# Kernel optimization log

Measured on AMD Instinct MI355X. Metric: run time of the kernel, lower is better.

The kernel has to match this reference:

```python
import jax, jax.numpy as jnp
import numpy as np

N, D = 8192, 512


def setup_inputs() -> dict:
    key = jax.random.key(0)
    ks = jax.random.split(key, 4)
    scale = 1.0 / np.sqrt(D)
    x = jax.random.normal(ks[0], (N, D), dtype=jnp.float32)
    Wq = jax.random.normal(ks[1], (D, D), dtype=jnp.float32) * scale
    Wk = jax.random.normal(ks[2], (D, D), dtype=jnp.float32) * scale
    Wv = jax.random.normal(ks[3], (D, D), dtype=jnp.float32) * scale
    bq = jnp.zeros((D,), dtype=jnp.float32)
    bk = jnp.zeros((D,), dtype=jnp.float32)
    bv = jnp.zeros((D,), dtype=jnp.float32)
    # causal additive mask: 0 on/below diagonal, -1e9 above
    mask = jnp.where(jnp.arange(N)[:, None] >= jnp.arange(N)[None, :], 0.0, -1e9).astype(jnp.float32)
    return {"x": x, "mask": mask, "Wq": Wq, "bq": bq, "Wk": Wk, "bk": bk, "Wv": Wv, "bv": bv}


def reference(x, mask, Wq, bq, Wk, bk, Wv, bv):
    # torch Linear: y = x @ W.T + b
    q = x @ Wq.T + bq  # [N, D]
    k = x @ Wk.T + bk  # [N, D]
    v = x @ Wv.T + bv  # [N, D]
    inv_sqrt_d = 1.0 / jnp.sqrt(jnp.asarray(D, dtype=x.dtype))
    scores = q @ k.T * inv_sqrt_d + mask          # [N, N] -- the HBM-heavy intermediate
    attention = jax.nn.softmax(scores, axis=-1)   # softmax over key axis
    weighted = attention @ v                       # [N, D]
    return weighted
```

## Files before the change

### kernel.cpp

```cpp
#include <hip/hip_runtime.h>
#include <hip/hip_bf16.h>
#include <stdint.h>


#define N_TOK 8192
#define DIM   512
#define NQB   128
#define CCH   12
#define MAXCH 11
#define NCHTOT 748

typedef __attribute__((ext_vector_type(8))) short bfrag;
typedef __attribute__((ext_vector_type(4))) float facc;
typedef __attribute__((ext_vector_type(4))) unsigned short us4v;
typedef __attribute__((ext_vector_type(2))) float f32x2v;

#define MFMA16(a, b, c) __builtin_amdgcn_mfma_f32_16x16x32_bf16((a), (b), (c), 0, 0, 0)

__device__ __forceinline__ unsigned short f2bf(float f) {
    union { float f; unsigned int u; } v; v.f = f;
    unsigned int r = v.u + 0x7fffu + ((v.u >> 16) & 1u);
    return (unsigned short)(r >> 16);
}
__device__ __forceinline__ float bf2f(unsigned int bits16) {
    union { unsigned int u; float f; } v; v.u = bits16 << 16;
    return v.f;
}
__device__ __forceinline__ void cp16(const unsigned short* g, const unsigned short* l) {
    __builtin_amdgcn_global_load_lds(
        (const __attribute__((address_space(1))) void*)g,
        (__attribute__((address_space(3))) void*)l, 16, 0, 0);
}

__device__ __forceinline__ int part_idx(int qb, int c) {
    return qb + 122 * c - 6 * c * c;
}

__global__ void cvt_x_kernel(const float* __restrict__ src,
                             unsigned short* __restrict__ dst, int n4) {
    int i = blockIdx.x * blockDim.x + threadIdx.x;
    if (i >= n4) return;
    float4 v = ((const float4*)src)[i];
    us4v o; o[0] = f2bf(v.x); o[1] = f2bf(v.y); o[2] = f2bf(v.z); o[3] = f2bf(v.w);
    ((us4v*)dst)[i] = o;
}

__global__ void cvt_w_kernel(const float* __restrict__ wq,
                             const float* __restrict__ wk,
                             const float* __restrict__ wv,
                             unsigned short* __restrict__ dst) {
    int i = blockIdx.x * blockDim.x + threadIdx.x;
    int g = i >> 16;
    int o = i & 65535;
    const float* s = (g == 0) ? wq : (g == 1) ? wk : wv;
    float4 v = ((const float4*)s)[o];
    us4v p; p[0] = f2bf(v.x); p[1] = f2bf(v.y); p[2] = f2bf(v.z); p[3] = f2bf(v.w);
    ((us4v*)dst)[i] = p;
}

__global__ __launch_bounds__(256, 2) void qkv_gemm(
    const unsigned short* __restrict__ xb,
    const unsigned short* __restrict__ wb,
    const float* __restrict__ biasq, const float* __restrict__ biask,
    const float* __restrict__ biasv,
    unsigned short* __restrict__ Qb, unsigned short* __restrict__ Kb,
    unsigned short* __restrict__ VTb) {
    const int z    = blockIdx.z;
    const int tid  = threadIdx.x;
    const int lane = tid & 63;
    const int w    = tid >> 6;
    const int wr   = w >> 1, wc = w & 1;
    const int r0   = blockIdx.x * 128;
    const int c0   = blockIdx.y * 128;
    const unsigned short* wmat = wb + z * 262144;
    const float* bias = (z == 0) ? biasq : (z == 1) ? biask : biasv;
    const int lr  = lane & 15;
    const int lkc = lane >> 4;

    __shared__ unsigned short AB[2][2][128 * 64];

    const int st_row = w * 8 + (lane >> 3);
    const int st_gs  = ((lane & 7) ^ (lane >> 3)) * 8;
    auto stage = [&](int step, int buf) {
        const int kb = step * 64;
#pragma unroll
        for (int i = 0; i < 4; ++i) {
            const int r = i * 32 + st_row;
            cp16(xb   + (size_t)(r0 + r) * 512 + kb + st_gs,
                 &AB[0][buf][(i * 256 + w * 64) * 8]);
            cp16(wmat + (size_t)(c0 + r) * 512 + kb + st_gs,
                 &AB[1][buf][(i * 256 + w * 64) * 8]);
        }
    };

    facc acc[4][4] = {};
    stage(0, 0);
    __syncthreads();

    int buf = 0;
    for (int step = 0; step < 8; ++step) {
        if (step + 1 < 8) stage(step + 1, buf ^ 1);
        bfrag af[4][2], bf4[4][2];
#pragma unroll
        for (int i = 0; i < 4; ++i) {
            const int m = wr * 64 + i * 16 + lr;
            const int mb = m * 64, m7 = m & 7;
            af[i][0] = *(const bfrag*)&AB[0][buf][mb + ((lkc) ^ m7) * 8];
            af[i][1] = *(const bfrag*)&AB[0][buf][mb + ((4 + lkc) ^ m7) * 8];
        }
#pragma unroll
        for (int j = 0; j < 4; ++j) {
            const int n = wc * 64 + j * 16 + lr;
            const int nb = n * 64, n7 = n & 7;
            bf4[j][0] = *(const bfrag*)&AB[1][buf][nb + ((lkc) ^ n7) * 8];
            bf4[j][1] = *(const bfrag*)&AB[1][buf][nb + ((4 + lkc) ^ n7) * 8];
        }
#pragma unroll
        for (int kk = 0; kk < 2; ++kk)
#pragma unroll
            for (int i = 0; i < 4; ++i)
#pragma unroll
                for (int j = 0; j < 4; ++j)
                    acc[i][j] = MFMA16(af[i][kk], bf4[j][kk], acc[i][j]);
        __syncthreads();
        buf ^= 1;
    }

    if (z < 2) {
        unsigned short* out = (z == 0) ? Qb : Kb;
#pragma unroll
        for (int i = 0; i < 4; ++i)
#pragma unroll
            for (int j = 0; j < 4; ++j) {
                const int col = c0 + wc * 64 + j * 16 + lr;
                const float bv_ = bias[col];
#pragma unroll
                for (int r = 0; r < 4; ++r) {
                    const int row = r0 + wr * 64 + i * 16 + lkc * 4 + r;
                    out[(size_t)row * 512 + col] = f2bf(acc[i][j][r] + bv_);
                }
            }
    } else {
#pragma unroll
        for (int i = 0; i < 4; ++i)
#pragma unroll
            for (int j = 0; j < 4; ++j) {
                const int col = c0 + wc * 64 + j * 16 + lr;
                const float bv_ = bias[col];
                us4v pk;
#pragma unroll
                for (int r = 0; r < 4; ++r) pk[r] = f2bf(acc[i][j][r] + bv_);
                *(us4v*)(VTb + (size_t)col * 8192 + (r0 + wr * 64 + i * 16 + lkc * 4)) = pk;
            }
    }
}

__global__ __launch_bounds__(512, 2) void attn_partial(
    const unsigned short* __restrict__ Qb, const unsigned short* __restrict__ Kb,
    const unsigned short* __restrict__ VTb,
    unsigned short* __restrict__ Opart, float* __restrict__ ml) {
    const int hb   = blockIdx.x;
    const int xcd  = hb & 7, pos = hb >> 3;
    const int idx  = (xcd < 4 ? xcd * 94 : 376 + (xcd - 4) * 93) + pos;
    int c = 0;
#pragma unroll
    for (int cc = 1; cc < MAXCH; ++cc)
        if (idx >= 134 * cc - 6 * cc * cc) c = cc;
    const int qb  = 12 * c + (idx - (134 * c - 6 * c * c));
    const int kb0 = c * CCH;
    const int kb1 = min(kb0 + CCH, qb + 1);

    const int tid  = threadIdx.x;
    const int lane = tid & 63;
    const int wv   = tid >> 6;
    const int sr   = wv & 3;
    const int ch   = wv >> 2;
    const int lr   = lane & 15;
    const int lkc  = lane >> 4;
    const int lk   = lkc * 8;
    const int qrow0 = qb * 64;

    __shared__ unsigned short Klds[2][64 * 512];
    __shared__ float          S_lds[64][65];
    __shared__ unsigned short P_lds[64][72];
    __shared__ float m_lds[64], l_lds[64], sc_lds[64];

    if (tid < 64) { m_lds[tid] = -1e30f; l_lds[tid] = 0.f; }

    auto stage_k = [&](int kb, int buf) {
        const unsigned short* src = Kb + (size_t)kb * (64 * 512) + (lane ^ wv) * 8;
#pragma unroll
        for (int i = 0; i < 8; ++i) {
            const int rl = wv + 8 * i;
            cp16(src + (size_t)rl * 512, &Klds[buf][rl * 512]);
        }
    };

    bfrag q[16];
    {
        const unsigned short* qp = Qb + (size_t)(qrow0 + sr * 16 + lr) * 512 + lk;
#pragma unroll
        for (int s = 0; s < 16; ++s) q[s] = *(const bfrag*)(qp + s * 32);
    }
    facc o[4][4] = {};
    stage_k(kb0, 0);
    __syncthreads();

    const int row = tid >> 3;
    const int sub = tid & 7;
    const float sm_scale = 0.044194173824159216f;
    int cur = 0;

    for (int kb = kb0; kb < kb1; ++kb) {
        const int cb = kb * 64;
        if (kb + 1 < kb1) stage_k(kb + 1, cur ^ 1);
        bfrag vbf[2][4];
#pragma unroll
        for (int s = 0; s < 2; ++s)
#pragma unroll
            for (int j = 0; j < 4; ++j)
                vbf[s][j] = *(const bfrag*)(VTb + (size_t)(wv * 64 + j * 16 + lr) * 8192
                                            + cb + s * 32 + lk);
#pragma unroll
        for (int tc = 0; tc < 2; ++tc) {
            facc sa0 = {}, sa1 = {};
            const int rl = ch * 32 + tc * 16 + lr;
            const unsigned short* kbase = &Klds[cur][rl * 512];
            const int rx = rl & 7;
#pragma unroll
            for (int s = 0; s < 16; s += 2) {
                const int sl0 = (s * 4 + lkc) ^ rx;
                const int sl1 = ((s + 1) * 4 + lkc) ^ rx;
                sa0 = MFMA16(q[s],     *(const bfrag*)(kbase + sl0 * 8), sa0);
                sa1 = MFMA16(q[s + 1], *(const bfrag*)(kbase + sl1 * 8), sa1);
            }
#pragma unroll
            for (int r = 0; r < 4; ++r)
                S_lds[sr * 16 + lkc * 4 + r][ch * 32 + tc * 16 + lr] = sa0[r] + sa1[r];
        }
        __syncthreads();

        {
            const int grow  = qrow0 + row;
            const bool diag = (kb == qb);
            float sv[8];
#pragma unroll
            for (int j = 0; j < 8; ++j) {
                float v = S_lds[row][sub * 8 + j] * sm_scale;
                if (diag && (cb + sub * 8 + j > grow)) v = -1e30f;
                sv[j] = v;
            }
            float mx = sv[0];
#pragma unroll
            for (int j = 1; j < 8; ++j) mx = fmaxf(mx, sv[j]);
            mx = fmaxf(mx, __shfl_xor(mx, 1));
            mx = fmaxf(mx, __shfl_xor(mx, 2));
            mx = fmaxf(mx, __shfl_xor(mx, 4));
            const float m_old = m_lds[row];
            const float m_new = fmaxf(m_old, mx);
            float sum = 0.f;
            bfrag pv_;
#pragma unroll
            for (int j = 0; j < 8; ++j) {
                float p = __expf(sv[j] - m_new);
                sum += p;
                pv_[j] = (short)f2bf(p);
            }
            sum += __shfl_xor(sum, 1);
            sum += __shfl_xor(sum, 2);
            sum += __shfl_xor(sum, 4);
            if (sub == 0) {
                const float scl = __expf(m_old - m_new);
                sc_lds[row] = scl;
                m_lds[row]  = m_new;
                l_lds[row]  = l_lds[row] * scl + sum;
            }
            *(bfrag*)(&P_lds[row][sub * 8]) = pv_;
        }
        __syncthreads();

#pragma unroll
        for (int i = 0; i < 4; ++i) {
            float s0 = sc_lds[i * 16 + lkc * 4 + 0];
            float s1 = sc_lds[i * 16 + lkc * 4 + 1];
            float s2 = sc_lds[i * 16 + lkc * 4 + 2];
            float s3 = sc_lds[i * 16 + lkc * 4 + 3];
#pragma unroll
            for (int j = 0; j < 4; ++j) {
                o[i][j][0] *= s0; o[i][j][1] *= s1;
                o[i][j][2] *= s2; o[i][j][3] *= s3;
            }
        }
#pragma unroll
        for (int s = 0; s < 2; ++s) {
            bfrag pa[4];
#pragma unroll
            for (int i = 0; i < 4; ++i)
                pa[i] = *(const bfrag*)(&P_lds[i * 16 + lr][s * 32 + lk]);
#pragma unroll
            for (int i = 0; i < 4; ++i)
#pragma unroll
                for (int j = 0; j < 4; ++j)
                    o[i][j] = MFMA16(pa[i], vbf[s][j], o[i][j]);
        }
        cur ^= 1;
    }

    {
        const size_t obase = (size_t)idx * (64 * 512);
#pragma unroll
        for (int i = 0; i < 4; ++i)
#pragma unroll
            for (int j = 0; j < 4; ++j) {
                const int colb = wv * 64 + j * 16 + lr;
#pragma unroll
                for (int r = 0; r < 4; ++r) {
                    const int rrow = i * 16 + lkc * 4 + r;
                    Opart[obase + (size_t)rrow * 512 + colb] = f2bf(o[i][j][r]);
                }
            }
        if (tid < 64) {
            ml[(size_t)idx * 128 + tid * 2 + 0] = m_lds[tid];
            ml[(size_t)idx * 128 + tid * 2 + 1] = l_lds[tid];
        }
    }
}

__global__ __launch_bounds__(256) void combine_k(
    const unsigned short* __restrict__ Opart, const float* __restrict__ ml,
    float* __restrict__ out) {
    const int qb  = blockIdx.x;
    const int rg  = blockIdx.y;
    const int nch = qb / 12 + 1;
    const int tid = threadIdx.x;
    __shared__ float wts[MAXCH][8];

    if (tid < 8) {
        const int lrow = rg * 8 + tid;
        float M = -1e30f;
        for (int cc = 0; cc < nch; ++cc)
            M = fmaxf(M, ml[(size_t)part_idx(qb, cc) * 128 + lrow * 2]);
        float den = 0.f;
        for (int cc = 0; cc < nch; ++cc) {
            float mc = ml[(size_t)part_idx(qb, cc) * 128 + lrow * 2];
            float lc = ml[(size_t)part_idx(qb, cc) * 128 + lrow * 2 + 1];
            den += lc * __expf(mc - M);
        }
        const float inv = 1.f / den;
#pragma unroll
        for (int cc = 0; cc < MAXCH; ++cc)
            wts[cc][tid] = (cc < nch)
                ? __expf(ml[(size_t)part_idx(qb, cc) * 128 + lrow * 2] - M) * inv
                : 0.f;
    }
    __syncthreads();

    float a0[8] = {}, a1[8] = {};
#pragma unroll
    for (int cc = 0; cc < MAXCH; ++cc) {
        const size_t base = (size_t)part_idx(qb, cc) * (64 * 512);
#pragma unroll
        for (int r = 0; r < 8; ++r) {
            const unsigned int pk = *(const unsigned int*)(
                Opart + base + (size_t)(rg * 8 + r) * 512 + tid * 2);
            const float w = wts[cc][r];
            a0[r] += w * bf2f(pk & 0xffffu);
            a1[r] += w * bf2f(pk >> 16);
        }
    }
#pragma unroll
    for (int r = 0; r < 8; ++r) {
        f32x2v res; res[0] = a0[r]; res[1] = a1[r];
        *(f32x2v*)(out + (size_t)(qb * 64 + rg * 8 + r) * 512 + tid * 2) = res;
    }
}

extern "C" void kernel_launch(void* const* d_in, const int* in_sizes, int n_in,
                              void* d_out, int out_size, void* d_ws, size_t ws_size,
                              hipStream_t stream) {
    const float* x  = (const float*)d_in[0];
    const float* Wq = (const float*)d_in[2];
    const float* bq = (const float*)d_in[3];
    const float* Wk = (const float*)d_in[4];
    const float* bk = (const float*)d_in[5];
    const float* Wv = (const float*)d_in[6];
    const float* bv = (const float*)d_in[7];
    float* out = (float*)d_out;

    char* ws = (char*)d_ws;
    unsigned short* xb  = (unsigned short*)(ws);
    unsigned short* Wb  = (unsigned short*)(ws + 8388608);
    unsigned short* Qb  = (unsigned short*)(ws + 9961472);
    unsigned short* Kb  = (unsigned short*)(ws + 18350080);
    unsigned short* VTb = (unsigned short*)(ws + 26738688);
    unsigned short* Op  = (unsigned short*)(ws + 35127296);
    float*          mlp = (float*)(ws + 84148224);

    hipLaunchKernelGGL(cvt_x_kernel, dim3(4096), dim3(256), 0, stream, x, xb, 1048576);
    hipLaunchKernelGGL(cvt_w_kernel, dim3(768), dim3(256), 0, stream, Wq, Wk, Wv, Wb);
    hipLaunchKernelGGL(qkv_gemm, dim3(64, 4, 3), dim3(256), 0, stream,
                       xb, Wb, bq, bk, bv, Qb, Kb, VTb);
    hipLaunchKernelGGL(attn_partial, dim3(NCHTOT), dim3(512), 0, stream,
                       Qb, Kb, VTb, Op, mlp);
    hipLaunchKernelGGL(combine_k, dim3(NQB, 8), dim3(256), 0, stream, Op, mlp, out);
}
```

Before: 478.5 us.

## Fuse Q/K/V projections into one GEMM sharing x tiles, add MFMA priority hints

Replaces the three-way z-indexed QKV GEMM with a single kernel. Each 512-thread block loads one x tile and computes the matching 128-column tiles of Q, K and V together, so x is read from global memory once instead of three times. The launch drops to 256 blocks, remapped so consecutive tiles spread across XCDs. s_setprio hints are wrapped around the MFMA bursts in both the GEMM and the attention kernel, and the P_lds row stride is padded from 72 to 80. The risks are fewer blocks than CUs, lower occupancy from the larger LDS footprint, and more register pressure.

```diff
diff --git a/kernel.cpp b/kernel.cpp
--- a/kernel.cpp
+++ b/kernel.cpp
@@ -58,100 +58,111 @@
     ((us4v*)dst)[i] = p;
 }
 
-__global__ __launch_bounds__(256, 2) void qkv_gemm(
+__global__ __launch_bounds__(512, 1) void qkv_fused(
     const unsigned short* __restrict__ xb,
     const unsigned short* __restrict__ wb,
     const float* __restrict__ biasq, const float* __restrict__ biask,
     const float* __restrict__ biasv,
     unsigned short* __restrict__ Qb, unsigned short* __restrict__ Kb,
     unsigned short* __restrict__ VTb) {
-    const int z    = blockIdx.z;
-    const int tid  = threadIdx.x;
-    const int lane = tid & 63;
-    const int w    = tid >> 6;
-    const int wr   = w >> 1, wc = w & 1;
-    const int r0   = blockIdx.x * 128;
-    const int c0   = blockIdx.y * 128;
-    const unsigned short* wmat = wb + z * 262144;
-    const float* bias = (z == 0) ? biasq : (z == 1) ? biask : biasv;
-    const int lr  = lane & 15;
-    const int lkc = lane >> 4;
-
-    __shared__ unsigned short AB[2][2][128 * 64];
+    const int bid = blockIdx.x;
+    const int idx = (bid & 7) * 32 + (bid >> 3);
+    const int bx = idx >> 2, by = idx & 3;
+    const int r0 = bx * 128, c0 = by * 128;
+    const int tid = threadIdx.x, lane = tid & 63, w = tid >> 6;
+    const int wm = w >> 2, wn = w & 3;
+    const int lr = lane & 15, lkc = lane >> 4;
+
+    __shared__ unsigned short A_lds[2][128 * 64];
+    __shared__ unsigned short B_lds[2][3][128 * 64];
 
     const int st_row = w * 8 + (lane >> 3);
     const int st_gs  = ((lane & 7) ^ (lane >> 3)) * 8;
     auto stage = [&](int step, int buf) {
         const int kb = step * 64;
 #pragma unroll
-        for (int i = 0; i < 4; ++i) {
-            const int r = i * 32 + st_row;
-            cp16(xb   + (size_t)(r0 + r) * 512 + kb + st_gs,
-                 &AB[0][buf][(i * 256 + w * 64) * 8]);
-            cp16(wmat + (size_t)(c0 + r) * 512 + kb + st_gs,
-                 &AB[1][buf][(i * 256 + w * 64) * 8]);
+        for (int i = 0; i < 2; ++i) {
+            const int r = i * 64 + st_row;
+            cp16(xb + (size_t)(r0 + r) * 512 + kb + st_gs,
+                 &A_lds[buf][(i * 512 + w * 64) * 8]);
+#pragma unroll
+            for (int z = 0; z < 3; ++z)
+                cp16(wb + (size_t)z * 262144 + (size_t)(c0 + r) * 512 + kb + st_gs,
+                     &B_lds[buf][z][(i * 512 + w * 64) * 8]);
         }
     };
 
-    facc acc[4][4] = {};
+    facc acc[3][4][2] = {};
     stage(0, 0);
     __syncthreads();
 
     int buf = 0;
     for (int step = 0; step < 8; ++step) {
         if (step + 1 < 8) stage(step + 1, buf ^ 1);
-        bfrag af[4][2], bf4[4][2];
+        bfrag af[4][2];
 #pragma unroll
         for (int i = 0; i < 4; ++i) {
-            const int m = wr * 64 + i * 16 + lr;
-            const int mb = m * 64, m7 = m & 7;
-            af[i][0] = *(const bfrag*)&AB[0][buf][mb + ((lkc) ^ m7) * 8];
-            af[i][1] = *(const bfrag*)&AB[0][buf][mb + ((4 + lkc) ^ m7) * 8];
-        }
-#pragma unroll
-        for (int j = 0; j < 4; ++j) {
-            const int n = wc * 64 + j * 16 + lr;
-            const int nb = n * 64, n7 = n & 7;
-            bf4[j][0] = *(const bfrag*)&AB[1][buf][nb + ((lkc) ^ n7) * 8];
-            bf4[j][1] = *(const bfrag*)&AB[1][buf][nb + ((4 + lkc) ^ n7) * 8];
-        }
-#pragma unroll
-        for (int kk = 0; kk < 2; ++kk)
-#pragma unroll
-            for (int i = 0; i < 4; ++i)
-#pragma unroll
-                for (int j = 0; j < 4; ++j)
-                    acc[i][j] = MFMA16(af[i][kk], bf4[j][kk], acc[i][j]);
+            const int m = wm * 64 + i * 16 + lr;
+            const int m7 = m & 7;
+#pragma unroll
+            for (int kk = 0; kk < 2; ++kk)
+                af[i][kk] = *(const bfrag*)&A_lds[buf][(m * 8 + ((kk * 4 + lkc) ^ m7)) * 8];
+        }
+#pragma unroll
+        for (int z = 0; z < 3; ++z) {
+            bfrag bf[2][2];
+#pragma unroll
+            for (int j = 0; j < 2; ++j) {
+                const int n = wn * 32 + j * 16 + lr;
+                const int n7 = n & 7;
+#pragma unroll
+                for (int kk = 0; kk < 2; ++kk)
+                    bf[j][kk] = *(const bfrag*)&B_lds[buf][z][(n * 8 + ((kk * 4 + lkc) ^ n7)) * 8];
+            }
+            __builtin_amdgcn_s_setprio(1);
+#pragma unroll
+            for (int kk = 0; kk < 2; ++kk)
+#pragma unroll
+                for (int i = 0; i < 4; ++i)
+#pragma unroll
+                    for (int j = 0; j < 2; ++j)
+                        acc[z][i][j] = MFMA16(af[i][kk], bf[j][kk], acc[z][i][j]);
+            __builtin_amdgcn_s_setprio(0);
+        }
         __syncthreads();
         buf ^= 1;
     }
 
-    if (z < 2) {
-        unsigned short* out = (z == 0) ? Qb : Kb;
-#pragma unroll
-        for (int i = 0; i < 4; ++i)
-#pragma unroll
-            for (int j = 0; j < 4; ++j) {
-                const int col = c0 + wc * 64 + j * 16 + lr;
-                const float bv_ = bias[col];
-#pragma unroll
-                for (int r = 0; r < 4; ++r) {
-                    const int row = r0 + wr * 64 + i * 16 + lkc * 4 + r;
-                    out[(size_t)row * 512 + col] = f2bf(acc[i][j][r] + bv_);
+#pragma unroll
+    for (int z = 0; z < 3; ++z) {
+        const float* bias = (z == 0) ? biasq : (z == 1) ? biask : biasv;
+        if (z < 2) {
+            unsigned short* out = (z == 0) ? Qb : Kb;
+#pragma unroll
+            for (int i = 0; i < 4; ++i)
+#pragma unroll
+                for (int j = 0; j < 2; ++j) {
+                    const int col = c0 + wn * 32 + j * 16 + lr;
+                    const float bv_ = bias[col];
+#pragma unroll
+                    for (int r = 0; r < 4; ++r) {
+                        const int row = r0 + wm * 64 + i * 16 + lkc * 4 + r;
+                        out[(size_t)row * 512 + col] = f2bf(acc[z][i][j][r] + bv_);
+                    }
                 }
-            }
-    } else {
-#pragma unroll
-        for (int i = 0; i < 4; ++i)
-#pragma unroll
-            for (int j = 0; j < 4; ++j) {
-                const int col = c0 + wc * 64 + j * 16 + lr;
-                const float bv_ = bias[col];
-                us4v pk;
-#pragma unroll
-                for (int r = 0; r < 4; ++r) pk[r] = f2bf(acc[i][j][r] + bv_);
-                *(us4v*)(VTb + (size_t)col * 8192 + (r0 + wr * 64 + i * 16 + lkc * 4)) = pk;
-            }
+        } else {
+#pragma unroll
+            for (int i = 0; i < 4; ++i)
+#pragma unroll
+                for (int j = 0; j < 2; ++j) {
+                    const int col = c0 + wn * 32 + j * 16 + lr;
+                    const float bv_ = bias[col];
+                    us4v pk;
+#pragma unroll
+                    for (int r = 0; r < 4; ++r) pk[r] = f2bf(acc[z][i][j][r] + bv_);
+                    *(us4v*)(VTb + (size_t)col * 8192 + (r0 + wm * 64 + i * 16 + lkc * 4)) = pk;
+                }
+        }
     }
 }
 
@@ -182,7 +193,7 @@
 
     __shared__ unsigned short Klds[2][64 * 512];
     __shared__ float          S_lds[64][65];
-    __shared__ unsigned short P_lds[64][72];
+    __shared__ unsigned short P_lds[64][80];
     __shared__ float m_lds[64], l_lds[64], sc_lds[64];
 
     if (tid < 64) { m_lds[tid] = -1e30f; l_lds[tid] = 0.f; }
@@ -227,6 +238,7 @@
             const int rl = ch * 32 + tc * 16 + lr;
             const unsigned short* kbase = &Klds[cur][rl * 512];
             const int rx = rl & 7;
+            __builtin_amdgcn_s_setprio(1);
 #pragma unroll
             for (int s = 0; s < 16; s += 2) {
                 const int sl0 = (s * 4 + lkc) ^ rx;
@@ -234,6 +246,7 @@
                 sa0 = MFMA16(q[s],     *(const bfrag*)(kbase + sl0 * 8), sa0);
                 sa1 = MFMA16(q[s + 1], *(const bfrag*)(kbase + sl1 * 8), sa1);
             }
+            __builtin_amdgcn_s_setprio(0);
 #pragma unroll
             for (int r = 0; r < 4; ++r)
                 S_lds[sr * 16 + lkc * 4 + r][ch * 32 + tc * 16 + lr] = sa0[r] + sa1[r];
@@ -297,11 +310,13 @@
 #pragma unroll
             for (int i = 0; i < 4; ++i)
                 pa[i] = *(const bfrag*)(&P_lds[i * 16 + lr][s * 32 + lk]);
+            __builtin_amdgcn_s_setprio(1);
 #pragma unroll
             for (int i = 0; i < 4; ++i)
 #pragma unroll
                 for (int j = 0; j < 4; ++j)
                     o[i][j] = MFMA16(pa[i], vbf[s][j], o[i][j]);
+            __builtin_amdgcn_s_setprio(0);
         }
         cur ^= 1;
     }
@@ -398,7 +413,7 @@
 
     hipLaunchKernelGGL(cvt_x_kernel, dim3(4096), dim3(256), 0, stream, x, xb, 1048576);
     hipLaunchKernelGGL(cvt_w_kernel, dim3(768), dim3(256), 0, stream, Wq, Wk, Wv, Wb);
-    hipLaunchKernelGGL(qkv_gemm, dim3(64, 4, 3), dim3(256), 0, stream,
+    hipLaunchKernelGGL(qkv_fused, dim3(256), dim3(512), 0, stream,
                        xb, Wb, bq, bk, bv, Qb, Kb, VTb);
     hipLaunchKernelGGL(attn_partial, dim3(NCHTOT), dim3(512), 0, stream,
                        Qb, Kb, VTb, Op, mlp);
```

New measurement: 518.9 us. 8.4% more time.
